# Performance work log

Measured on AMD Instinct MI355X. Metric: run time of the kernel, lower is better.

The kernel has to match this reference:

```python
import jax, jax.numpy as jnp
import numpy as np

M_MOL = 8192      # number of molecules
A_ATOMS = 32      # atoms per molecule (uniform ragged groups)
N_FEAT = 128      # schnet n_atom_basis


def setup_inputs() -> dict:
    key = jax.random.key(0)
    sr = jax.random.normal(key, (M_MOL * A_ATOMS, N_FEAT), dtype=jnp.float32)
    # idx_m: sorted molecule index per atom, uniform group sizes
    idx_m = jnp.repeat(jnp.arange(M_MOL, dtype=jnp.int32), A_ATOMS)
    return {"scalar_representation": sr, "idx_m": idx_m}


def reference(scalar_representation, idx_m):
    # maxm = int(idx_m[-1]) + 1 in the torch code; groups are uniform here so
    # torch.split over bincount == a simple reshape into [M, A, F].
    maxm = int(idx_m[-1]) + 1
    n_atoms = scalar_representation.shape[0]
    a = n_atoms // maxm
    sr = scalar_representation.reshape(maxm, a, -1)          # [M, A, F]
    # per-molecule correlation (Gram) matrix: c = sr @ sr.T
    c = jnp.einsum('maf,mbf->mab', sr, sr)                    # [M, A, A]
    # eigvalsh returns ascending eigenvalues; torch code takes [0] (smallest)
    eigvals = jnp.linalg.eigvalsh(c)                          # [M, A]
    return eigvals[:, 0]                                      # [M]
```

## Files before the change

kernel.cpp:

```cpp
#include <hip/hip_runtime.h>
#include <hip/hip_bf16.h>

#define DEVINL __device__ __forceinline__

typedef __attribute__((ext_vector_type(8))) short short8;
typedef __attribute__((ext_vector_type(4))) float f32x4;

DEVINL float rcp_f(float x) { return __builtin_amdgcn_rcpf(x); }

#define LDS_FENCE() __asm__ volatile("" ::: "memory")

DEVINL short bf_hi(float f, float& rem) {
  unsigned u = __float_as_uint(f);
  unsigned rh = (u + 0x8000u) >> 16;
  rem = f - __uint_as_float(rh << 16);
  return (short)rh;
}
DEVINL short bf_of(float f) {
  return (short)((__float_as_uint(f) + 0x8000u) >> 16);
}
DEVINL void cvt_hilo(float4 fa, float4 fb, short8& h, short8& lo) {
  float rm;
  h[0] = bf_hi(fa.x, rm); lo[0] = bf_of(rm);
  h[1] = bf_hi(fa.y, rm); lo[1] = bf_of(rm);
  h[2] = bf_hi(fa.z, rm); lo[2] = bf_of(rm);
  h[3] = bf_hi(fa.w, rm); lo[3] = bf_of(rm);
  h[4] = bf_hi(fb.x, rm); lo[4] = bf_of(rm);
  h[5] = bf_hi(fb.y, rm); lo[5] = bf_of(rm);
  h[6] = bf_hi(fb.z, rm); lo[6] = bf_of(rm);
  h[7] = bf_hi(fb.w, rm); lo[7] = bf_of(rm);
}
DEVINL f32x4 mfma_bf16(short8 a, short8 b, f32x4 c) {
  return __builtin_amdgcn_mfma_f32_16x16x32_bf16(a, b, c, 0, 0, 0);
}

template<int K>
DEVINL void house_step(float (&r)[32], int l,
                       float* vbuf, float* pbuf, float* dbuf, float* ebuf) {
  constexpr int C0 = (K + 1) / 4;
  constexpr int PE = (K + 1) & 3;

  float xm = (l > K) ? r[K] : 0.0f;
  vbuf[l] = xm;
  LDS_FENCE();

  float4 vc[8];
  #pragma unroll
  for (int c = 0; c < 8; ++c) vc[c] = make_float4(0.f, 0.f, 0.f, 0.f);
  #pragma unroll
  for (int c = C0; c < 8; ++c) vc[c] = *(const float4*)(vbuf + 4 * c);

  float x0;
  if constexpr (PE == 0)      x0 = vc[C0].x;
  else if constexpr (PE == 1) x0 = vc[C0].y;
  else if constexpr (PE == 2) x0 = vc[C0].z;
  else                        x0 = vc[C0].w;

  float n0 = 0.0f, n1 = 0.0f;
  #pragma unroll
  for (int c = C0; c < 8; ++c) {
    n0 = fmaf(vc[c].x, vc[c].x, n0); n1 = fmaf(vc[c].y, vc[c].y, n1);
    n0 = fmaf(vc[c].z, vc[c].z, n0); n1 = fmaf(vc[c].w, vc[c].w, n1);
  }
  float nn = n0 + n1;

  float alpha = -copysignf(sqrtf(nn), x0);
  float denom = nn - alpha * x0;
  float beta = (denom > 1e-20f) ? rcp_f(denom) : 0.0f;

  float v = xm - ((l == K + 1) ? alpha : 0.0f);
  if constexpr (PE == 0)      vc[C0].x -= alpha;
  else if constexpr (PE == 1) vc[C0].y -= alpha;
  else if constexpr (PE == 2) vc[C0].z -= alpha;
  else                        vc[C0].w -= alpha;

  float a0 = 0.0f, a1 = 0.0f;
  #pragma unroll
  for (int c = C0; c < 8; ++c) {
    a0 = fmaf(r[4 * c + 0], vc[c].x, a0); a1 = fmaf(r[4 * c + 1], vc[c].y, a1);
    a0 = fmaf(r[4 * c + 2], vc[c].z, a0); a1 = fmaf(r[4 * c + 3], vc[c].w, a1);
  }
  float p = a0 + a1;

  pbuf[l] = p;
  LDS_FENCE();

  float bv = beta * v;
  float bp = (l > K) ? beta * p : 0.0f;

  float g0 = 0.0f, g1 = 0.0f;
  #pragma unroll
  for (int c = C0; c < 8; ++c) {
    float4 pcx = *(const float4*)(pbuf + 4 * c);
    g0 = fmaf(vc[c].x, pcx.x, g0); g1 = fmaf(vc[c].y, pcx.y, g1);
    g0 = fmaf(vc[c].z, pcx.z, g0); g1 = fmaf(vc[c].w, pcx.w, g1);
    r[4 * c + 0] -= bv * pcx.x + bp * vc[c].x;
    r[4 * c + 1] -= bv * pcx.y + bp * vc[c].y;
    r[4 * c + 2] -= bv * pcx.z + bp * vc[c].z;
    r[4 * c + 3] -= bv * pcx.w + bp * vc[c].w;
  }
  float G = g0 + g1;
  float tv = (beta * beta * G) * v;

  #pragma unroll
  for (int c = C0; c < 8; ++c) {
    r[4 * c + 0] = fmaf(tv, vc[c].x, r[4 * c + 0]);
    r[4 * c + 1] = fmaf(tv, vc[c].y, r[4 * c + 1]);
    r[4 * c + 2] = fmaf(tv, vc[c].z, r[4 * c + 2]);
    r[4 * c + 3] = fmaf(tv, vc[c].w, r[4 * c + 3]);
  }

  if (l == K) { dbuf[K] = r[K]; ebuf[K] = alpha; }
}

template<int K>
DEVINL void house_all(float (&r)[32], int l,
                      float* vbuf, float* pbuf, float* dbuf, float* ebuf) {
  house_step<K>(r, l, vbuf, pbuf, dbuf, ebuf);
  if constexpr (K < 30) house_all<K + 1>(r, l, vbuf, pbuf, dbuf, ebuf);
}

__global__ __launch_bounds__(256) void Correlation_85134841741354_kernel(
    const float* __restrict__ A, float* __restrict__ out, int M) {
  const int lane = threadIdx.x & 63;
  const int wave = threadIdx.x >> 6;
  const int q    = lane >> 4;
  const int t    = lane & 15;
  const int a    = lane >> 5;
  const int l    = lane & 31;
  const int molbase = blockIdx.x * 8 + wave * 2;
  if (molbase >= M) return;

  __shared__ float ldsT[4][2][32 * 36 + 8];

  #pragma unroll 1
  for (int g = 0; g < 2; ++g) {
    const float* Am = A + (size_t)(molbase + g) * (32 * 128);
    f32x4 acc00 = {0.f, 0.f, 0.f, 0.f}, acc01 = {0.f, 0.f, 0.f, 0.f};
    f32x4 acc10 = {0.f, 0.f, 0.f, 0.f}, acc11 = {0.f, 0.f, 0.f, 0.f};
    #pragma unroll
    for (int c = 0; c < 4; ++c) {
      const float* pr0 = Am + t * 128        + 32 * c + 8 * q;
      const float* pr1 = Am + (t + 16) * 128 + 32 * c + 8 * q;
      float4 fa0 = *(const float4*)(pr0);
      float4 fb0 = *(const float4*)(pr0 + 4);
      float4 fa1 = *(const float4*)(pr1);
      float4 fb1 = *(const float4*)(pr1 + 4);
      short8 h0, l0, h1, l1;
      cvt_hilo(fa0, fb0, h0, l0);
      cvt_hilo(fa1, fb1, h1, l1);
      acc00 = mfma_bf16(h0, h0, acc00); acc00 = mfma_bf16(h0, l0, acc00); acc00 = mfma_bf16(l0, h0, acc00);
      acc01 = mfma_bf16(h0, h1, acc01); acc01 = mfma_bf16(h0, l1, acc01); acc01 = mfma_bf16(l0, h1, acc01);
      acc10 = mfma_bf16(h1, h0, acc10); acc10 = mfma_bf16(h1, l0, acc10); acc10 = mfma_bf16(l1, h0, acc10);
      acc11 = mfma_bf16(h1, h1, acc11); acc11 = mfma_bf16(h1, l1, acc11); acc11 = mfma_bf16(l1, h1, acc11);
    }
    float* tg = &ldsT[wave][g][0];
    #pragma unroll
    for (int reg = 0; reg < 4; ++reg) {
      tg[(4 * q + reg) * 36 + t]           = acc00[reg];
      tg[(4 * q + reg) * 36 + 16 + t]      = acc01[reg];
      tg[(16 + 4 * q + reg) * 36 + t]      = acc10[reg];
      tg[(16 + 4 * q + reg) * 36 + 16 + t] = acc11[reg];
    }
  }
  LDS_FENCE();

  float* tq = &ldsT[wave][a][0];
  float r[32];
  #pragma unroll
  for (int c = 0; c < 8; ++c) {
    float4 x = *(const float4*)(tq + l * 36 + 4 * c);
    r[4 * c + 0] = x.x; r[4 * c + 1] = x.y;
    r[4 * c + 2] = x.z; r[4 * c + 3] = x.w;
  }
  LDS_FENCE();

  float* vbuf = tq;
  float* pbuf = tq + 40;
  float* dbuf = tq + 80;
  float* ebuf = tq + 120;

  house_all<0>(r, l, vbuf, pbuf, dbuf, ebuf);
  if (l == 31) { dbuf[31] = r[31]; ebuf[31] = 0.0f; }
  LDS_FENCE();

  float vd[32], ve[32];
  #pragma unroll
  for (int c = 0; c < 8; ++c) {
    float4 dc = *(const float4*)(dbuf + 4 * c);
    float4 ec = *(const float4*)(ebuf + 4 * c);
    vd[4 * c + 0] = dc.x; vd[4 * c + 1] = dc.y;
    vd[4 * c + 2] = dc.z; vd[4 * c + 3] = dc.w;
    ve[4 * c + 0] = ec.x; ve[4 * c + 1] = ec.y;
    ve[4 * c + 2] = ec.z; ve[4 * c + 3] = ec.w;
  }
  float glo = vd[0] - fabsf(ve[0]);
  float ghi = vd[0] + fabsf(ve[0]);
  #pragma unroll
  for (int i = 1; i < 32; ++i) {
    float rad = fabsf(ve[i]) + fabsf(ve[i - 1]);
    glo = fminf(glo, vd[i] - rad);
    ghi = fmaxf(ghi, vd[i] + rad);
  }
  float lo = fmaxf(glo - 1e-3f, 0.0f);
  float hi = ghi + 1e-3f;

  #pragma unroll
  for (int i = 0; i < 32; ++i) ve[i] *= ve[i];

  #pragma unroll
  for (int rr = 0; rr < 3; ++rr) {
    float stp = (hi - lo) * (1.0f / 33.0f);
    float sig = fmaf(stp, (float)(l + 1), lo);
    float qq = vd[0] - sig;
    int cnt = (qq < 0.0f) ? 1 : 0;
    #pragma unroll
    for (int i = 1; i < 32; ++i) {
      float qs = (fabsf(qq) < 1e-12f) ? ((qq < 0.0f) ? -1e-12f : 1e-12f) : qq;
      qq = (vd[i] - sig) - ve[i - 1] * rcp_f(qs);
      cnt += (qq < 0.0f) ? 1 : 0;
    }
    unsigned long long m64 = __ballot(cnt >= 1);
    unsigned hm = (unsigned)(m64 >> (a * 32));
    int b = (hm == 0u) ? 32 : (__ffs(hm) - 1);
    float nhi = (b == 32) ? hi : fmaf(stp, (float)(b + 1), lo);
    lo = fmaf(stp, (float)b, lo);
    hi = nhi;
  }

  if (l == 0) out[molbase + a] = 0.5f * (lo + hi);
}

extern "C" void kernel_launch(void* const* d_in, const int* in_sizes, int n_in,
                              void* d_out, int out_size, void* d_ws, size_t ws_size,
                              hipStream_t stream) {
  const float* A = (const float*)d_in[0];
  float* out = (float*)d_out;
  int n_atoms = in_sizes[1];
  int M = n_atoms / 32;
  int blocks = (M + 7) / 8;
  hipLaunchKernelGGL(Correlation_85134841741354_kernel,
                     dim3(blocks), dim3(256), 0, stream, A, out, M);
}
```

Before: 220.7 us.

## Split into gram, Householder, and Sturm kernels with two lanes per row

Splits the fused kernel into three launches: the Gram matrix goes to a workspace, a Householder tridiagonalization kernel runs one molecule per wave with two lanes per row (16 registers each, partial sums combined via DPP), and a separate bisection kernel reads the diagonal and off-diagonal. This halves per-lane register pressure and serial work in the tridiagonalization and uses all 64 lanes on one molecule. In exchange it adds two launches and a 32 MB workspace round trip through global memory.

```diff
diff --git a/kernel.cpp b/kernel.cpp
--- a/kernel.cpp
+++ b/kernel.cpp
@@ -9,6 +9,13 @@
 DEVINL float rcp_f(float x) { return __builtin_amdgcn_rcpf(x); }
 
 #define LDS_FENCE() __asm__ volatile("" ::: "memory")
+
+template<int CTRL>
+DEVINL float dpp_mov(float x) {
+  return __int_as_float(__builtin_amdgcn_update_dpp(
+      0, __float_as_int(x), CTRL, 0xF, 0xF, true));
+}
+DEVINL float pair_sum(float x) { return x + dpp_mov<0xB1>(x); }
 
 DEVINL short bf_hi(float f, float& rem) {
   unsigned u = __float_as_uint(f);
@@ -34,94 +41,8 @@
   return __builtin_amdgcn_mfma_f32_16x16x32_bf16(a, b, c, 0, 0, 0);
 }
 
-template<int K>
-DEVINL void house_step(float (&r)[32], int l,
-                       float* vbuf, float* pbuf, float* dbuf, float* ebuf) {
-  constexpr int C0 = (K + 1) / 4;
-  constexpr int PE = (K + 1) & 3;
-
-  float xm = (l > K) ? r[K] : 0.0f;
-  vbuf[l] = xm;
-  LDS_FENCE();
-
-  float4 vc[8];
-  #pragma unroll
-  for (int c = 0; c < 8; ++c) vc[c] = make_float4(0.f, 0.f, 0.f, 0.f);
-  #pragma unroll
-  for (int c = C0; c < 8; ++c) vc[c] = *(const float4*)(vbuf + 4 * c);
-
-  float x0;
-  if constexpr (PE == 0)      x0 = vc[C0].x;
-  else if constexpr (PE == 1) x0 = vc[C0].y;
-  else if constexpr (PE == 2) x0 = vc[C0].z;
-  else                        x0 = vc[C0].w;
-
-  float n0 = 0.0f, n1 = 0.0f;
-  #pragma unroll
-  for (int c = C0; c < 8; ++c) {
-    n0 = fmaf(vc[c].x, vc[c].x, n0); n1 = fmaf(vc[c].y, vc[c].y, n1);
-    n0 = fmaf(vc[c].z, vc[c].z, n0); n1 = fmaf(vc[c].w, vc[c].w, n1);
-  }
-  float nn = n0 + n1;
-
-  float alpha = -copysignf(sqrtf(nn), x0);
-  float denom = nn - alpha * x0;
-  float beta = (denom > 1e-20f) ? rcp_f(denom) : 0.0f;
-
-  float v = xm - ((l == K + 1) ? alpha : 0.0f);
-  if constexpr (PE == 0)      vc[C0].x -= alpha;
-  else if constexpr (PE == 1) vc[C0].y -= alpha;
-  else if constexpr (PE == 2) vc[C0].z -= alpha;
-  else                        vc[C0].w -= alpha;
-
-  float a0 = 0.0f, a1 = 0.0f;
-  #pragma unroll
-  for (int c = C0; c < 8; ++c) {
-    a0 = fmaf(r[4 * c + 0], vc[c].x, a0); a1 = fmaf(r[4 * c + 1], vc[c].y, a1);
-    a0 = fmaf(r[4 * c + 2], vc[c].z, a0); a1 = fmaf(r[4 * c + 3], vc[c].w, a1);
-  }
-  float p = a0 + a1;
-
-  pbuf[l] = p;
-  LDS_FENCE();
-
-  float bv = beta * v;
-  float bp = (l > K) ? beta * p : 0.0f;
-
-  float g0 = 0.0f, g1 = 0.0f;
-  #pragma unroll
-  for (int c = C0; c < 8; ++c) {
-    float4 pcx = *(const float4*)(pbuf + 4 * c);
-    g0 = fmaf(vc[c].x, pcx.x, g0); g1 = fmaf(vc[c].y, pcx.y, g1);
-    g0 = fmaf(vc[c].z, pcx.z, g0); g1 = fmaf(vc[c].w, pcx.w, g1);
-    r[4 * c + 0] -= bv * pcx.x + bp * vc[c].x;
-    r[4 * c + 1] -= bv * pcx.y + bp * vc[c].y;
-    r[4 * c + 2] -= bv * pcx.z + bp * vc[c].z;
-    r[4 * c + 3] -= bv * pcx.w + bp * vc[c].w;
-  }
-  float G = g0 + g1;
-  float tv = (beta * beta * G) * v;
-
-  #pragma unroll
-  for (int c = C0; c < 8; ++c) {
-    r[4 * c + 0] = fmaf(tv, vc[c].x, r[4 * c + 0]);
-    r[4 * c + 1] = fmaf(tv, vc[c].y, r[4 * c + 1]);
-    r[4 * c + 2] = fmaf(tv, vc[c].z, r[4 * c + 2]);
-    r[4 * c + 3] = fmaf(tv, vc[c].w, r[4 * c + 3]);
-  }
-
-  if (l == K) { dbuf[K] = r[K]; ebuf[K] = alpha; }
-}
-
-template<int K>
-DEVINL void house_all(float (&r)[32], int l,
-                      float* vbuf, float* pbuf, float* dbuf, float* ebuf) {
-  house_step<K>(r, l, vbuf, pbuf, dbuf, ebuf);
-  if constexpr (K < 30) house_all<K + 1>(r, l, vbuf, pbuf, dbuf, ebuf);
-}
-
-__global__ __launch_bounds__(256) void Correlation_85134841741354_kernel(
-    const float* __restrict__ A, float* __restrict__ out, int M) {
+__global__ __launch_bounds__(256) void gram_kernel(
+    const float* __restrict__ A, float* __restrict__ W, int M) {
   const int lane = threadIdx.x & 63;
   const int wave = threadIdx.x >> 6;
   const int q    = lane >> 4;
@@ -165,30 +86,138 @@
   }
   LDS_FENCE();
 
-  float* tq = &ldsT[wave][a][0];
-  float r[32];
+  const float* tq = &ldsT[wave][a][0];
+  float* Wm = W + (size_t)(molbase + a) * 1024;
   #pragma unroll
   for (int c = 0; c < 8; ++c) {
     float4 x = *(const float4*)(tq + l * 36 + 4 * c);
-    r[4 * c + 0] = x.x; r[4 * c + 1] = x.y;
-    r[4 * c + 2] = x.z; r[4 * c + 3] = x.w;
-  }
+    *(float4*)(Wm + (c * 32 + l) * 4) = x;
+  }
+}
+
+template<int K>
+DEVINL void house_step(float (&r)[16], int row, int h,
+                       float* vbuf, float* pbuf, float* de) {
+  constexpr int HK = K >> 4, EK = K & 15;
+  constexpr int HP = (K + 1) >> 4, PE = (K + 1) & 15;
+  constexpr int PC = PE >> 2, PEE = PE & 3;
+
+  float xm = (row > K) ? r[EK] : 0.0f;
+  if (h == HK) vbuf[row] = xm;
   LDS_FENCE();
 
-  float* vbuf = tq;
-  float* pbuf = tq + 40;
-  float* dbuf = tq + 80;
-  float* ebuf = tq + 120;
-
-  house_all<0>(r, l, vbuf, pbuf, dbuf, ebuf);
-  if (l == 31) { dbuf[31] = r[31]; ebuf[31] = 0.0f; }
+  float4 vc[4];
+  #pragma unroll
+  for (int j = 0; j < 4; ++j) vc[j] = *(const float4*)(vbuf + 16 * h + 4 * j);
+  float x_me = vbuf[row];
+  float x0   = vbuf[K + 1];
+
+  float n0 = 0.f, n1 = 0.f;
+  #pragma unroll
+  for (int j = 0; j < 4; ++j) {
+    n0 = fmaf(vc[j].x, vc[j].x, n0); n1 = fmaf(vc[j].y, vc[j].y, n1);
+    n0 = fmaf(vc[j].z, vc[j].z, n0); n1 = fmaf(vc[j].w, vc[j].w, n1);
+  }
+  float nn = pair_sum(n0 + n1);
+
+  float alpha = -copysignf(sqrtf(nn), x0);
+  float denom = nn - alpha * x0;
+  float beta  = (denom > 1e-20f) ? rcp_f(denom) : 0.0f;
+  float v_me  = x_me - ((row == K + 1) ? alpha : 0.0f);
+
+  if (h == HP) {
+    if constexpr (PEE == 0)      vc[PC].x -= alpha;
+    else if constexpr (PEE == 1) vc[PC].y -= alpha;
+    else if constexpr (PEE == 2) vc[PC].z -= alpha;
+    else                         vc[PC].w -= alpha;
+  }
+
+  float a0 = 0.f, a1 = 0.f;
+  #pragma unroll
+  for (int j = 0; j < 4; ++j) {
+    a0 = fmaf(r[4 * j + 0], vc[j].x, a0); a1 = fmaf(r[4 * j + 1], vc[j].y, a1);
+    a0 = fmaf(r[4 * j + 2], vc[j].z, a0); a1 = fmaf(r[4 * j + 3], vc[j].w, a1);
+  }
+  float p_me = pair_sum(a0 + a1);
+  if (h == 0) pbuf[row] = p_me;
   LDS_FENCE();
 
+  float bv = beta * v_me;
+  float bp = (row > K) ? beta * p_me : 0.0f;
+
+  float g0 = 0.f, g1 = 0.f;
+  #pragma unroll
+  for (int j = 0; j < 4; ++j) {
+    float4 pcx = *(const float4*)(pbuf + 16 * h + 4 * j);
+    g0 = fmaf(vc[j].x, pcx.x, g0); g1 = fmaf(vc[j].y, pcx.y, g1);
+    g0 = fmaf(vc[j].z, pcx.z, g0); g1 = fmaf(vc[j].w, pcx.w, g1);
+    r[4 * j + 0] -= bv * pcx.x + bp * vc[j].x;
+    r[4 * j + 1] -= bv * pcx.y + bp * vc[j].y;
+    r[4 * j + 2] -= bv * pcx.z + bp * vc[j].z;
+    r[4 * j + 3] -= bv * pcx.w + bp * vc[j].w;
+  }
+  float G  = pair_sum(g0 + g1);
+  float tv = (beta * beta * G) * v_me;
+
+  #pragma unroll
+  for (int j = 0; j < 4; ++j) {
+    r[4 * j + 0] = fmaf(tv, vc[j].x, r[4 * j + 0]);
+    r[4 * j + 1] = fmaf(tv, vc[j].y, r[4 * j + 1]);
+    r[4 * j + 2] = fmaf(tv, vc[j].z, r[4 * j + 2]);
+    r[4 * j + 3] = fmaf(tv, vc[j].w, r[4 * j + 3]);
+  }
+
+  if (row == K && h == HK) { de[K] = r[EK]; de[32 + K] = alpha; }
+}
+
+template<int K>
+DEVINL void house_all(float (&r)[16], int row, int h,
+                      float* vbuf, float* pbuf, float* de) {
+  house_step<K>(r, row, h, vbuf, pbuf, de);
+  if constexpr (K < 30) house_all<K + 1>(r, row, h, vbuf, pbuf, de);
+}
+
+__global__ __launch_bounds__(256) void house_kernel(
+    const float* __restrict__ W, float* __restrict__ DE, int M) {
+  const int lane = threadIdx.x & 63;
+  const int wave = threadIdx.x >> 6;
+  const int row  = lane >> 1;
+  const int h    = lane & 1;
+  const int mol  = blockIdx.x * 4 + wave;
+  if (mol >= M) return;
+
+  __shared__ float sc[4][72];
+  float* vbuf = &sc[wave][0];
+  float* pbuf = &sc[wave][36];
+
+  const float* Wm = W + (size_t)mol * 1024;
+  float r[16];
+  #pragma unroll
+  for (int j = 0; j < 4; ++j) {
+    float4 x = *(const float4*)(Wm + ((4 * h + j) * 32 + row) * 4);
+    r[4 * j + 0] = x.x; r[4 * j + 1] = x.y;
+    r[4 * j + 2] = x.z; r[4 * j + 3] = x.w;
+  }
+
+  float* de = DE + (size_t)mol * 64;
+  house_all<0>(r, row, h, vbuf, pbuf, de);
+  if (row == 31 && h == 1) { de[31] = r[15]; de[63] = 0.0f; }
+}
+
+__global__ __launch_bounds__(256) void sturm_kernel(
+    const float* __restrict__ DE, float* __restrict__ out, int M) {
+  const int lane = threadIdx.x & 63;
+  const int wave = threadIdx.x >> 6;
+  const int a = lane >> 5, l = lane & 31;
+  const int mol = blockIdx.x * 8 + wave * 2 + a;
+  if (mol >= M) return;
+
+  const float* dm = DE + (size_t)mol * 64;
   float vd[32], ve[32];
   #pragma unroll
   for (int c = 0; c < 8; ++c) {
-    float4 dc = *(const float4*)(dbuf + 4 * c);
-    float4 ec = *(const float4*)(ebuf + 4 * c);
+    float4 dc = *(const float4*)(dm + 4 * c);
+    float4 ec = *(const float4*)(dm + 32 + 4 * c);
     vd[4 * c + 0] = dc.x; vd[4 * c + 1] = dc.y;
     vd[4 * c + 2] = dc.z; vd[4 * c + 3] = dc.w;
     ve[4 * c + 0] = ec.x; ve[4 * c + 1] = ec.y;
@@ -228,7 +257,7 @@
     hi = nhi;
   }
 
-  if (l == 0) out[molbase + a] = 0.5f * (lo + hi);
+  if (l == 0) out[mol] = 0.5f * (lo + hi);
 }
 
 extern "C" void kernel_launch(void* const* d_in, const int* in_sizes, int n_in,
@@ -238,7 +267,9 @@
   float* out = (float*)d_out;
   int n_atoms = in_sizes[1];
   int M = n_atoms / 32;
-  int blocks = (M + 7) / 8;
-  hipLaunchKernelGGL(Correlation_85134841741354_kernel,
-                     dim3(blocks), dim3(256), 0, stream, A, out, M);
-}
+  float* W  = (float*)d_ws;
+  float* DE = W + (size_t)M * 1024;
+  hipLaunchKernelGGL(gram_kernel,  dim3(M / 8), dim3(256), 0, stream, A, W, M);
+  hipLaunchKernelGGL(house_kernel, dim3(M / 4), dim3(256), 0, stream, W, DE, M);
+  hipLaunchKernelGGL(sturm_kernel, dim3(M / 8), dim3(256), 0, stream, DE, out, M);
+}
```

Result: slower. 253.5 us (+14.8%).
